# Optimization experiments

Measured on AMD Instinct MI355X. Metric: run time of the kernel, lower is better.

Reference implementation:

```python
import jax, jax.numpy as jnp
import numpy as np

B, T, E, H = 8, 1024, 128, 8
S = E // H  # 16, narrow per-head dim


def setup_inputs() -> dict:
    key = jax.random.key(0)
    ks = jax.random.split(key, 7)
    return {
        "x": jax.random.normal(ks[0], (B, T, E), dtype=jnp.float32),
        "masks": jax.random.randint(ks[1], (B, T), 0, 2, dtype=jnp.int32),
        "Wq": jax.random.normal(ks[2], (S, S), dtype=jnp.float32) * 0.05,
        "Wk": jax.random.normal(ks[3], (S, S), dtype=jnp.float32) * 0.05,
        "Wv": jax.random.normal(ks[4], (S, S), dtype=jnp.float32) * 0.05,
        "Wu": jax.random.normal(ks[5], (E, E), dtype=jnp.float32) * 0.05,
        "bu": jnp.zeros((E,), dtype=jnp.float32),
        "temporal_only": 1,
    }


def reference(x, masks, Wq, Wk, Wv, Wu, bu, temporal_only):
    b, t, e = x.shape
    h = H
    s = e // h
    x4 = x.reshape(b, t, h, s)
    # nn.Linear(s, s, bias=False): y = x @ W.T, applied per head
    q = jnp.einsum('bths,ds->bthd', x4, Wq)
    k = jnp.einsum('bths,ds->bthd', x4, Wk)
    v = jnp.einsum('bths,ds->bthd', x4, Wv)
    scale = jnp.float32(e) ** 0.25
    q = q / scale
    k = k / scale
    # (b, h, t, t) attention logits
    dot = jnp.einsum('bqhd,bkhd->bhqk', q, k)
    # temporal_only masking: masks is (b, t), applied on key axis then query axis
    m = masks.astype(bool)
    neg = jnp.float32(-1e9)
    dot = jnp.where(m[:, None, None, :], dot, neg)
    dot = jnp.where(m[:, None, :, None], dot, neg)
    attn = jax.nn.softmax(dot, axis=-1)
    # post-softmax zeroing with the same masks
    attn = jnp.where(m[:, None, None, :], attn, jnp.float32(0.0))
    attn = jnp.where(m[:, None, :, None], attn, jnp.float32(0.0))
    out = jnp.einsum('bhqk,bkhd->bqhd', attn, v).reshape(b, t, h * s)
    return out @ Wu.T + bu
```

## Files before the change

kernel.cpp:

```cpp
#include <hip/hip_runtime.h>

#define NB 8
#define NT 1024
#define NE 128
#define NH 8
#define NS 16

#define WS_Q 0
#define WS_K 1048576
#define WS_V 2097152
#define WS_Y 3145728
#define WS_VIDX 4194304

#define WT_PITCH 132

static __device__ __forceinline__ void fma4(float4& acc, float s, const float4 v) {
  acc.x = fmaf(s, v.x, acc.x);
  acc.y = fmaf(s, v.y, acc.y);
  acc.z = fmaf(s, v.z, acc.z);
  acc.w = fmaf(s, v.w, acc.w);
}

static __device__ __forceinline__ float dot16(const float4 x0, const float4 x1,
                                              const float4 x2, const float4 x3,
                                              const float4 w0, const float4 w1,
                                              const float4 w2, const float4 w3) {
  float s0 = (x0.x * w0.x + x0.y * w0.y) + (x0.z * w0.z + x0.w * w0.w);
  float s1 = (x1.x * w1.x + x1.y * w1.y) + (x1.z * w1.z + x1.w * w1.w);
  float s2 = (x2.x * w2.x + x2.y * w2.y) + (x2.z * w2.z + x2.w * w2.w);
  float s3 = (x3.x * w3.x + x3.y * w3.y) + (x3.z * w3.z + x3.w * w3.w);
  return (s0 + s1) + (s2 + s3);
}

__global__ __launch_bounds__(256) void qkv_kernel(
    const float* __restrict__ x, const int* __restrict__ masks,
    const float* __restrict__ Wq, const float* __restrict__ Wk,
    const float* __restrict__ Wv, float* __restrict__ Q, float* __restrict__ K,
    float* __restrict__ V, int* __restrict__ vidx, int* __restrict__ vcount) {
  if (blockIdx.x >= 1024) {
    const int b = blockIdx.x - 1024;
    const int lane = threadIdx.x;
    if (lane < 64) {
      int base = 0;
      for (int c = 0; c < NT; c += 64) {
        int t = c + lane;
        int v = masks[b * NT + t] != 0;
        unsigned long long bal = __ballot(v);
        int pos = base + __popcll(bal & ((1ull << lane) - 1ull));
        if (v) vidx[b * NT + pos] = t;
        base += __popcll(bal);
      }
      if (lane == 0) vcount[b] = base;
    }
    return;
  }
  const int tid = threadIdx.x;
  const int h = blockIdx.x & 7;
  const int rg = blockIdx.x >> 3;
  const int b = rg >> 4;
  const int base = rg << 6;
  const int d = tid & 15;
  const int r = base + ((tid >> 4) << 2);
  const float4* wq4 = (const float4*)(Wq + d * 16);
  const float4 wq0 = wq4[0], wq1 = wq4[1], wq2 = wq4[2], wq3 = wq4[3];
  const float4* wk4 = (const float4*)(Wk + d * 16);
  const float4 wk0 = wk4[0], wk1 = wk4[1], wk2 = wk4[2], wk3 = wk4[3];
  const float4* wv4 = (const float4*)(Wv + d * 16);
  const float4 wv0 = wv4[0], wv1 = wv4[1], wv2 = wv4[2], wv3 = wv4[3];
  const float invs = 0.08838834764831845f;
#pragma unroll
  for (int i = 0; i < 4; i++) {
    const int row = r + i;
    const float4* xp = (const float4*)(x + (size_t)row * 128 + h * 16);
    const float4 x0 = xp[0], x1 = xp[1], x2 = xp[2], x3 = xp[3];
    float aq = dot16(x0, x1, x2, x3, wq0, wq1, wq2, wq3);
    float ak = dot16(x0, x1, x2, x3, wk0, wk1, wk2, wk3);
    float av = dot16(x0, x1, x2, x3, wv0, wv1, wv2, wv3);
    const int t = row & 1023;
    size_t o = ((size_t)(b * NH + h) * NT + t) * NS + d;
    Q[o] = aq * invs;
    K[o] = ak;
    V[o] = av;
  }
}

__global__ __launch_bounds__(256) void attn_kernel(
    const float* __restrict__ Q, const float* __restrict__ K,
    const float* __restrict__ V, const int* __restrict__ masks,
    const int* __restrict__ vidx, const int* __restrict__ vcount,
    float* __restrict__ Y) {
  __shared__ __align__(16) float Ks[2048];
  __shared__ __align__(16) float Vs[2048];
  __shared__ __align__(16) float om[2][4][64][20];
  __shared__ float ml[2][4][64][2];
  const int tid = threadIdx.x;
  const int lane = tid & 63;
  const int split = tid >> 6;
  const int bh = blockIdx.x >> 3;
  const int b = bh >> 3, h = bh & 7;
  const int tbase = (blockIdx.x & 7) << 7;
  const int tA = tbase + lane;
  const int nv = vcount[b];
  const float4* qga = (const float4*)(Q + ((size_t)bh * NT + tA) * NS);
  const float4 qa0 = qga[0], qa1 = qga[1], qa2 = qga[2], qa3 = qga[3];
  const float4* qgb = (const float4*)(Q + ((size_t)bh * NT + tA + 64) * NS);
  const float4 qb0 = qgb[0], qb1 = qgb[1], qb2 = qgb[2], qb3 = qgb[3];
  float mA = -1e30f, lA = 0.f, mB = -1e30f, lB = 0.f;
  float4 oa0 = {0, 0, 0, 0}, oa1 = {0, 0, 0, 0}, oa2 = {0, 0, 0, 0},
         oa3 = {0, 0, 0, 0};
  float4 ob0 = {0, 0, 0, 0}, ob1 = {0, 0, 0, 0}, ob2 = {0, 0, 0, 0},
         ob3 = {0, 0, 0, 0};

  for (int k0 = 0; k0 < nv; k0 += 128) {
    __syncthreads();
    const int quad = tid & 3;
    const int jr = tid >> 2;
#pragma unroll
    for (int p = 0; p < 2; p++) {
      int row = jr + (p << 6);
      int j = k0 + row;
      float4 kv = {0, 0, 0, 0}, vv = {0, 0, 0, 0};
      if (j < nv) {
        int kk = vidx[b * NT + j];
        size_t bse = ((size_t)bh * NT + kk) * NS + (quad << 2);
        kv = *(const float4*)(K + bse);
        vv = *(const float4*)(V + bse);
      }
      *(float4*)(Ks + row * 16 + (quad << 2)) = kv;
      *(float4*)(Vs + row * 16 + (quad << 2)) = vv;
    }
    __syncthreads();
    int jmax = nv - k0;
    if (jmax > 128) jmax = 128;
    for (int g = 0; g < 8; g++) {
      const int rbase = split + (g << 4);
      if (rbase >= jmax) break;
      float sA[4], sB[4];
#pragma unroll
      for (int i = 0; i < 4; i++) {
        const float4* kr = (const float4*)(Ks + (rbase + (i << 2)) * 16);
        float4 k0v = kr[0], k1v = kr[1], k2v = kr[2], k3v = kr[3];
        sA[i] = dot16(qa0, qa1, qa2, qa3, k0v, k1v, k2v, k3v);
        sB[i] = dot16(qb0, qb1, qb2, qb3, k0v, k1v, k2v, k3v);
      }
#pragma unroll
      for (int i = 0; i < 4; i++)
        if (rbase + (i << 2) >= jmax) { sA[i] = -1e30f; sB[i] = -1e30f; }
      float mbA = fmaxf(fmaxf(sA[0], sA[1]), fmaxf(sA[2], sA[3]));
      if (mbA > mA) {
        float al = __expf(mA - mbA);
        lA *= al;
        oa0.x *= al; oa0.y *= al; oa0.z *= al; oa0.w *= al;
        oa1.x *= al; oa1.y *= al; oa1.z *= al; oa1.w *= al;
        oa2.x *= al; oa2.y *= al; oa2.z *= al; oa2.w *= al;
        oa3.x *= al; oa3.y *= al; oa3.z *= al; oa3.w *= al;
        mA = mbA;
      }
      float pA[4];
      pA[0] = __expf(sA[0] - mA); pA[1] = __expf(sA[1] - mA);
      pA[2] = __expf(sA[2] - mA); pA[3] = __expf(sA[3] - mA);
      lA += (pA[0] + pA[1]) + (pA[2] + pA[3]);
      float mbB = fmaxf(fmaxf(sB[0], sB[1]), fmaxf(sB[2], sB[3]));
      if (mbB > mB) {
        float al = __expf(mB - mbB);
        lB *= al;
        ob0.x *= al; ob0.y *= al; ob0.z *= al; ob0.w *= al;
        ob1.x *= al; ob1.y *= al; ob1.z *= al; ob1.w *= al;
        ob2.x *= al; ob2.y *= al; ob2.z *= al; ob2.w *= al;
        ob3.x *= al; ob3.y *= al; ob3.z *= al; ob3.w *= al;
        mB = mbB;
      }
      float pB[4];
      pB[0] = __expf(sB[0] - mB); pB[1] = __expf(sB[1] - mB);
      pB[2] = __expf(sB[2] - mB); pB[3] = __expf(sB[3] - mB);
      lB += (pB[0] + pB[1]) + (pB[2] + pB[3]);
#pragma unroll
      for (int i = 0; i < 4; i++) {
        const float4* vr = (const float4*)(Vs + (rbase + (i << 2)) * 16);
        float4 v0 = vr[0], v1 = vr[1], v2 = vr[2], v3 = vr[3];
        fma4(oa0, pA[i], v0); fma4(oa1, pA[i], v1);
        fma4(oa2, pA[i], v2); fma4(oa3, pA[i], v3);
        fma4(ob0, pB[i], v0); fma4(ob1, pB[i], v1);
        fma4(ob2, pB[i], v2); fma4(ob3, pB[i], v3);
      }
    }
  }
  ml[0][split][lane][0] = mA; ml[0][split][lane][1] = lA;
  ml[1][split][lane][0] = mB; ml[1][split][lane][1] = lB;
  {
    float* pa = &om[0][split][lane][0];
    *(float4*)(pa + 0) = oa0; *(float4*)(pa + 4) = oa1;
    *(float4*)(pa + 8) = oa2; *(float4*)(pa + 12) = oa3;
    float* pb = &om[1][split][lane][0];
    *(float4*)(pb + 0) = ob0; *(float4*)(pb + 4) = ob1;
    *(float4*)(pb + 8) = ob2; *(float4*)(pb + 12) = ob3;
  }
  __syncthreads();
  if (split < 2) {
    const int qg = split;
    const int tq = tbase + (qg << 6) + lane;
    float m0 = ml[qg][0][lane][0], l0 = ml[qg][0][lane][1];
    float m1 = ml[qg][1][lane][0], l1 = ml[qg][1][lane][1];
    float m2 = ml[qg][2][lane][0], l2 = ml[qg][2][lane][1];
    float m3 = ml[qg][3][lane][0], l3 = ml[qg][3][lane][1];
    float M = fmaxf(fmaxf(m0, m1), fmaxf(m2, m3));
    float f0 = __expf(m0 - M), f1 = __expf(m1 - M), f2 = __expf(m2 - M),
          f3 = __expf(m3 - M);
    float L = f0 * l0 + f1 * l1 + f2 * l2 + f3 * l3;
    float4 y0 = {0, 0, 0, 0}, y1 = {0, 0, 0, 0}, y2 = {0, 0, 0, 0},
           y3 = {0, 0, 0, 0};
    float fs[4] = {f0, f1, f2, f3};
#pragma unroll
    for (int s = 0; s < 4; s++) {
      const float* p = &om[qg][s][lane][0];
      fma4(y0, fs[s], *(const float4*)(p + 0));
      fma4(y1, fs[s], *(const float4*)(p + 4));
      fma4(y2, fs[s], *(const float4*)(p + 8));
      fma4(y3, fs[s], *(const float4*)(p + 12));
    }
    const int qm = masks[b * NT + tq];
    const float inv = (qm != 0 && L > 0.f) ? (1.0f / L) : 0.f;
    y0.x *= inv; y0.y *= inv; y0.z *= inv; y0.w *= inv;
    y1.x *= inv; y1.y *= inv; y1.z *= inv; y1.w *= inv;
    y2.x *= inv; y2.y *= inv; y2.z *= inv; y2.w *= inv;
    y3.x *= inv; y3.y *= inv; y3.z *= inv; y3.w *= inv;
    float4* yo = (float4*)(Y + ((size_t)b * NT + tq) * NE + h * NS);
    yo[0] = y0; yo[1] = y1; yo[2] = y2; yo[3] = y3;
  }
}

__global__ __launch_bounds__(256) void proj_kernel(
    const float* __restrict__ Y, const float* __restrict__ Wu,
    const float* __restrict__ bu, float* __restrict__ out) {
  __shared__ __align__(16) float Wt[64 * WT_PITCH];
  __shared__ __align__(16) float Yt[16 * 128];
  const int tid = threadIdx.x;
  const int r0 = blockIdx.x * 16;
  const float4* yg = (const float4*)(Y + (size_t)r0 * 128);
  float4* yt4 = (float4*)Yt;
  yt4[tid] = yg[tid];
  yt4[tid + 256] = yg[tid + 256];
  const int c0 = (tid & 31) << 2;
  const int rg = (tid >> 5) & 3;
  const int eh = tid >> 7;
  float4 acc0 = {0, 0, 0, 0}, acc1 = {0, 0, 0, 0}, acc2 = {0, 0, 0, 0},
         acc3 = {0, 0, 0, 0};
  for (int e0 = 0; e0 < 128; e0 += 64) {
    __syncthreads();
#pragma unroll
    for (int p = 0; p < 8; p++) {
      int idx = tid + p * 256;
      int c = idx >> 4;
      int es = (idx & 15) << 2;
      float4 w = *(const float4*)(Wu + c * 128 + e0 + es);
      Wt[(es + 0) * WT_PITCH + c] = w.x;
      Wt[(es + 1) * WT_PITCH + c] = w.y;
      Wt[(es + 2) * WT_PITCH + c] = w.z;
      Wt[(es + 3) * WT_PITCH + c] = w.w;
    }
    __syncthreads();
    const int eb = eh << 5;
    const float* y0 = Yt + (rg * 4 + 0) * 128 + e0 + eb;
    const float* y1 = Yt + (rg * 4 + 1) * 128 + e0 + eb;
    const float* y2 = Yt + (rg * 4 + 2) * 128 + e0 + eb;
    const float* y3 = Yt + (rg * 4 + 3) * 128 + e0 + eb;
#pragma unroll 4
    for (int e = 0; e < 32; e += 4) {
      const float* wb = Wt + (eb + e) * WT_PITCH + c0;
      float4 w0 = *(const float4*)(wb + 0 * WT_PITCH);
      float4 w1 = *(const float4*)(wb + 1 * WT_PITCH);
      float4 w2 = *(const float4*)(wb + 2 * WT_PITCH);
      float4 w3 = *(const float4*)(wb + 3 * WT_PITCH);
      float4 ya = *(const float4*)(y0 + e);
      float4 yb = *(const float4*)(y1 + e);
      float4 yc = *(const float4*)(y2 + e);
      float4 yd = *(const float4*)(y3 + e);
      fma4(acc0, ya.x, w0); fma4(acc0, ya.y, w1); fma4(acc0, ya.z, w2); fma4(acc0, ya.w, w3);
      fma4(acc1, yb.x, w0); fma4(acc1, yb.y, w1); fma4(acc1, yb.z, w2); fma4(acc1, yb.w, w3);
      fma4(acc2, yc.x, w0); fma4(acc2, yc.y, w1); fma4(acc2, yc.z, w2); fma4(acc2, yc.w, w3);
      fma4(acc3, yd.x, w0); fma4(acc3, yd.y, w1); fma4(acc3, yd.z, w2); fma4(acc3, yd.w, w3);
    }
  }
  __syncthreads();
  if (eh == 1) {
    float* p = Wt + (tid & 127) * 20;
    *(float4*)(p + 0) = acc0; *(float4*)(p + 4) = acc1;
    *(float4*)(p + 8) = acc2; *(float4*)(p + 12) = acc3;
  }
  __syncthreads();
  if (eh == 0) {
    const float* p = Wt + tid * 20;
    float4 b4 = *(const float4*)(bu + c0);
    float4 q0 = *(const float4*)(p + 0);
    float4 q1 = *(const float4*)(p + 4);
    float4 q2 = *(const float4*)(p + 8);
    float4 q3 = *(const float4*)(p + 12);
    acc0.x += q0.x + b4.x; acc0.y += q0.y + b4.y; acc0.z += q0.z + b4.z; acc0.w += q0.w + b4.w;
    acc1.x += q1.x + b4.x; acc1.y += q1.y + b4.y; acc1.z += q1.z + b4.z; acc1.w += q1.w + b4.w;
    acc2.x += q2.x + b4.x; acc2.y += q2.y + b4.y; acc2.z += q2.z + b4.z; acc2.w += q2.w + b4.w;
    acc3.x += q3.x + b4.x; acc3.y += q3.y + b4.y; acc3.z += q3.z + b4.z; acc3.w += q3.w + b4.w;
    *(float4*)(out + (size_t)(r0 + rg * 4 + 0) * 128 + c0) = acc0;
    *(float4*)(out + (size_t)(r0 + rg * 4 + 1) * 128 + c0) = acc1;
    *(float4*)(out + (size_t)(r0 + rg * 4 + 2) * 128 + c0) = acc2;
    *(float4*)(out + (size_t)(r0 + rg * 4 + 3) * 128 + c0) = acc3;
  }
}

extern "C" void kernel_launch(void* const* d_in, const int* in_sizes, int n_in,
                              void* d_out, int out_size, void* d_ws,
                              size_t ws_size, hipStream_t stream) {
  const float* x = (const float*)d_in[0];
  const int* masks = (const int*)d_in[1];
  const float* Wq = (const float*)d_in[2];
  const float* Wk = (const float*)d_in[3];
  const float* Wv = (const float*)d_in[4];
  const float* Wu = (const float*)d_in[5];
  const float* bu = (const float*)d_in[6];
  float* out = (float*)d_out;

  float* ws = (float*)d_ws;
  float* Q = ws + WS_Q;
  float* K = ws + WS_K;
  float* V = ws + WS_V;
  float* Y = ws + WS_Y;
  int* vidx = (int*)(ws + WS_VIDX);
  int* vcount = vidx + NB * NT;

  qkv_kernel<<<1024 + NB, 256, 0, stream>>>(x, masks, Wq, Wk, Wv, Q, K, V,
                                            vidx, vcount);
  attn_kernel<<<NB * NH * (NT / 128), 256, 0, stream>>>(Q, K, V, masks, vidx,
                                                        vcount, Y);
  proj_kernel<<<NB * NT / 16, 256, 0, stream>>>(Y, Wu, bu, out);
}
```

Before: 141.5 us.

## Split attention key range across eight waves per block with aliased shared memory merge

```diff
diff --git a/kernel.cpp b/kernel.cpp
--- a/kernel.cpp
+++ b/kernel.cpp
@@ -84,15 +84,14 @@
   }
 }
 
-__global__ __launch_bounds__(256) void attn_kernel(
+__global__ __launch_bounds__(512, 4) void attn_kernel(
     const float* __restrict__ Q, const float* __restrict__ K,
     const float* __restrict__ V, const int* __restrict__ masks,
     const int* __restrict__ vidx, const int* __restrict__ vcount,
     float* __restrict__ Y) {
-  __shared__ __align__(16) float Ks[2048];
-  __shared__ __align__(16) float Vs[2048];
-  __shared__ __align__(16) float om[2][4][64][20];
-  __shared__ float ml[2][4][64][2];
+  __shared__ __align__(16) float smem[10240];
+  float* Ks = smem;
+  float* Vs = smem + 2048;
   const int tid = threadIdx.x;
   const int lane = tid & 63;
   const int split = tid >> 6;
@@ -115,10 +114,8 @@
     __syncthreads();
     const int quad = tid & 3;
     const int jr = tid >> 2;
-#pragma unroll
-    for (int p = 0; p < 2; p++) {
-      int row = jr + (p << 6);
-      int j = k0 + row;
+    {
+      int j = k0 + jr;
       float4 kv = {0, 0, 0, 0}, vv = {0, 0, 0, 0};
       if (j < nv) {
         int kk = vidx[b * NT + j];
@@ -126,26 +123,26 @@
         kv = *(const float4*)(K + bse);
         vv = *(const float4*)(V + bse);
       }
-      *(float4*)(Ks + row * 16 + (quad << 2)) = kv;
-      *(float4*)(Vs + row * 16 + (quad << 2)) = vv;
+      *(float4*)(Ks + jr * 16 + (quad << 2)) = kv;
+      *(float4*)(Vs + jr * 16 + (quad << 2)) = vv;
     }
     __syncthreads();
     int jmax = nv - k0;
     if (jmax > 128) jmax = 128;
-    for (int g = 0; g < 8; g++) {
-      const int rbase = split + (g << 4);
+    for (int g = 0; g < 4; g++) {
+      const int rbase = split + (g << 5);
       if (rbase >= jmax) break;
       float sA[4], sB[4];
 #pragma unroll
       for (int i = 0; i < 4; i++) {
-        const float4* kr = (const float4*)(Ks + (rbase + (i << 2)) * 16);
+        const float4* kr = (const float4*)(Ks + (rbase + (i << 3)) * 16);
         float4 k0v = kr[0], k1v = kr[1], k2v = kr[2], k3v = kr[3];
         sA[i] = dot16(qa0, qa1, qa2, qa3, k0v, k1v, k2v, k3v);
         sB[i] = dot16(qb0, qb1, qb2, qb3, k0v, k1v, k2v, k3v);
       }
 #pragma unroll
       for (int i = 0; i < 4; i++)
-        if (rbase + (i << 2) >= jmax) { sA[i] = -1e30f; sB[i] = -1e30f; }
+        if (rbase + (i << 3) >= jmax) { sA[i] = -1e30f; sB[i] = -1e30f; }
       float mbA = fmaxf(fmaxf(sA[0], sA[1]), fmaxf(sA[2], sA[3]));
       if (mbA > mA) {
         float al = __expf(mA - mbA);
@@ -176,7 +173,7 @@
       lB += (pB[0] + pB[1]) + (pB[2] + pB[3]);
 #pragma unroll
       for (int i = 0; i < 4; i++) {
-        const float4* vr = (const float4*)(Vs + (rbase + (i << 2)) * 16);
+        const float4* vr = (const float4*)(Vs + (rbase + (i << 3)) * 16);
         float4 v0 = vr[0], v1 = vr[1], v2 = vr[2], v3 = vr[3];
         fma4(oa0, pA[i], v0); fma4(oa1, pA[i], v1);
         fma4(oa2, pA[i], v2); fma4(oa3, pA[i], v3);
@@ -185,38 +182,77 @@
       }
     }
   }
-  ml[0][split][lane][0] = mA; ml[0][split][lane][1] = lA;
-  ml[1][split][lane][0] = mB; ml[1][split][lane][1] = lB;
+  __syncthreads();
+  float* om = smem;
   {
-    float* pa = &om[0][split][lane][0];
+    float* pa = om + (split * 64 + lane) * 20;
     *(float4*)(pa + 0) = oa0; *(float4*)(pa + 4) = oa1;
     *(float4*)(pa + 8) = oa2; *(float4*)(pa + 12) = oa3;
-    float* pb = &om[1][split][lane][0];
+    pa[16] = mA; pa[17] = lA;
+  }
+  __syncthreads();
+  if (tid < 64) {
+    const int tq = tbase + tid;
+    float ms[8], ls[8];
+#pragma unroll
+    for (int s = 0; s < 8; s++) {
+      const float* p = om + (s * 64 + tid) * 20;
+      ms[s] = p[16]; ls[s] = p[17];
+    }
+    float M = fmaxf(fmaxf(fmaxf(ms[0], ms[1]), fmaxf(ms[2], ms[3])),
+                    fmaxf(fmaxf(ms[4], ms[5]), fmaxf(ms[6], ms[7])));
+    float L = 0.f;
+    float4 y0 = {0, 0, 0, 0}, y1 = {0, 0, 0, 0}, y2 = {0, 0, 0, 0},
+           y3 = {0, 0, 0, 0};
+#pragma unroll
+    for (int s = 0; s < 8; s++) {
+      float f = __expf(ms[s] - M);
+      L = fmaf(f, ls[s], L);
+      const float* p = om + (s * 64 + tid) * 20;
+      fma4(y0, f, *(const float4*)(p + 0));
+      fma4(y1, f, *(const float4*)(p + 4));
+      fma4(y2, f, *(const float4*)(p + 8));
+      fma4(y3, f, *(const float4*)(p + 12));
+    }
+    const int qm = masks[b * NT + tq];
+    const float inv = (qm != 0 && L > 0.f) ? (1.0f / L) : 0.f;
+    y0.x *= inv; y0.y *= inv; y0.z *= inv; y0.w *= inv;
+    y1.x *= inv; y1.y *= inv; y1.z *= inv; y1.w *= inv;
+    y2.x *= inv; y2.y *= inv; y2.z *= inv; y2.w *= inv;
+    y3.x *= inv; y3.y *= inv; y3.z *= inv; y3.w *= inv;
+    float4* yo = (float4*)(Y + ((size_t)b * NT + tq) * NE + h * NS);
+    yo[0] = y0; yo[1] = y1; yo[2] = y2; yo[3] = y3;
+  }
+  __syncthreads();
+  {
+    float* pb = om + (split * 64 + lane) * 20;
     *(float4*)(pb + 0) = ob0; *(float4*)(pb + 4) = ob1;
     *(float4*)(pb + 8) = ob2; *(float4*)(pb + 12) = ob3;
-  }
-  __syncthreads();
-  if (split < 2) {
-    const int qg = split;
-    const int tq = tbase + (qg << 6) + lane;
-    float m0 = ml[qg][0][lane][0], l0 = ml[qg][0][lane][1];
-    float m1 = ml[qg][1][lane][0], l1 = ml[qg][1][lane][1];
-    float m2 = ml[qg][2][lane][0], l2 = ml[qg][2][lane][1];
-    float m3 = ml[qg][3][lane][0], l3 = ml[qg][3][lane][1];
-    float M = fmaxf(fmaxf(m0, m1), fmaxf(m2, m3));
-    float f0 = __expf(m0 - M), f1 = __expf(m1 - M), f2 = __expf(m2 - M),
-          f3 = __expf(m3 - M);
-    float L = f0 * l0 + f1 * l1 + f2 * l2 + f3 * l3;
+    pb[16] = mB; pb[17] = lB;
+  }
+  __syncthreads();
+  if (tid < 64) {
+    const int tq = tbase + 64 + tid;
+    float ms[8], ls[8];
+#pragma unroll
+    for (int s = 0; s < 8; s++) {
+      const float* p = om + (s * 64 + tid) * 20;
+      ms[s] = p[16]; ls[s] = p[17];
+    }
+    float M = fmaxf(fmaxf(fmaxf(ms[0], ms[1]), fmaxf(ms[2], ms[3])),
+                    fmaxf(fmaxf(ms[4], ms[5]), fmaxf(ms[6], ms[7])));
+    float L = 0.f;
     float4 y0 = {0, 0, 0, 0}, y1 = {0, 0, 0, 0}, y2 = {0, 0, 0, 0},
            y3 = {0, 0, 0, 0};
-    float fs[4] = {f0, f1, f2, f3};
-#pragma unroll
-    for (int s = 0; s < 4; s++) {
-      const float* p = &om[qg][s][lane][0];
-      fma4(y0, fs[s], *(const float4*)(p + 0));
-      fma4(y1, fs[s], *(const float4*)(p + 4));
-      fma4(y2, fs[s], *(const float4*)(p + 8));
-      fma4(y3, fs[s], *(const float4*)(p + 12));
+#pragma unroll
+    for (int s = 0; s < 8; s++) {
+      float f = __expf(ms[s] - M);
+      L = fmaf(f, ls[s], L);
+      const float* p = om + (s * 64 + tid) * 20;
+      fma4(y0, f, *(const float4*)(p + 0));
+      fma4(y1, f, *(const float4*)(p + 4));
+      fma4(y2, f, *(const float4*)(p + 8));
+      fma4(y3, f, *(const float4*)(p + 12));
     }
     const int qm = masks[b * NT + tq];
     const float inv = (qm != 0 && L > 0.f) ? (1.0f / L) : 0.f;
@@ -328,7 +364,7 @@
 
   qkv_kernel<<<1024 + NB, 256, 0, stream>>>(x, masks, Wq, Wk, Wv, Q, K, V,
                                             vidx, vcount);
-  attn_kernel<<<NB * NH * (NT / 128), 256, 0, stream>>>(Q, K, V, masks, vidx,
+  attn_kernel<<<NB * NH * (NT / 128), 512, 0, stream>>>(Q, K, V, masks, vidx,
                                                         vcount, Y);
   proj_kernel<<<NB * NT / 16, 256, 0, stream>>>(Y, Wu, bu, out);
 }
```

Result: slower. 243.9 us (+72.4%).
